# Performance work log

Measured on AMD Instinct MI355X. Metric: run time of the kernel, lower is better.

## Reference

```python
import jax, jax.numpy as jnp
import numpy as np

EMBED_DIM = 768
NUM_HEADS = 12
HEAD_DIM = EMBED_DIM // NUM_HEADS
SCALE = HEAD_DIM ** -0.5


def setup_inputs() -> dict:
    key = jax.random.key(0)
    k_x, k_qw, k_qb, k_pw, k_pb = jax.random.split(key, 5)
    B, N, C = 8, 1024, EMBED_DIM
    std = C ** -0.5
    return {
        "x": jax.random.normal(k_x, (B, N, C), dtype=jnp.float32),
        "qkv_w": jax.random.normal(k_qw, (C, 3 * C), dtype=jnp.float32) * std,
        "qkv_b": jax.random.normal(k_qb, (3 * C,), dtype=jnp.float32) * 0.02,
        "proj_w": jax.random.normal(k_pw, (C, C), dtype=jnp.float32) * std,
        "proj_b": jax.random.normal(k_pb, (C,), dtype=jnp.float32) * 0.02,
    }


def reference(x, qkv_w, qkv_b, proj_w, proj_b):
    B, N, C = x.shape
    # QKV projection: [B,N,3C] -> [3,B,H,N,Dh]
    qkv = (x @ qkv_w + qkv_b).reshape(B, N, 3, NUM_HEADS, HEAD_DIM)
    qkv = jnp.transpose(qkv, (2, 0, 3, 1, 4))
    q, k, v = qkv[0], qkv[1], qkv[2]
    # attention scores [B,H,N,N]
    attn = jnp.einsum("bhqd,bhkd->bhqk", q, k) * SCALE
    attn_weights = jax.nn.softmax(attn, axis=-1)
    # dropout=0.0 (eval) -> identity
    out = jnp.einsum("bhqk,bhkd->bhqd", attn_weights, v)
    out = jnp.transpose(out, (0, 2, 1, 3)).reshape(B, N, C)
    out = out @ proj_w + proj_b
    return out, attn_weights
```

## Files before the change

kernel.cpp:

```cpp
#include <hip/hip_runtime.h>
#include <cstdint>
#include <cstddef>

namespace {

constexpr int B = 8, NSEQ = 1024, C = 768, H = 12, D = 64, N3 = 2304;
constexpr float SCALE = 0.125f;
constexpr size_t QKV_ELEMS = (size_t)B * H * NSEQ * D;

using f32x4 = __attribute__((ext_vector_type(4))) float;
using s16x8 = __attribute__((ext_vector_type(8))) short;

__device__ __forceinline__ unsigned short f2bf(float f) {
  union { float f; uint32_t u; } v; v.f = f;
  const uint32_t r = v.u + 0x7FFFu + ((v.u >> 16) & 1u);
  return (unsigned short)(r >> 16);
}
__device__ __forceinline__ float bf2f(unsigned short s) {
  union { uint32_t u; float f; } v; v.u = ((uint32_t)s) << 16;
  return v.f;
}
__device__ __forceinline__ void gload_lds16(const void* g, void* l) {
  __builtin_amdgcn_global_load_lds(
      (const __attribute__((address_space(1))) uint32_t*)g,
      (__attribute__((address_space(3))) uint32_t*)l, 16, 0, 0);
}

__global__ __launch_bounds__(256)
void cvt_x(const float* __restrict__ x, unsigned short* __restrict__ xb, int n4) {
  const int stride = gridDim.x * 256;
  for (int idx = blockIdx.x * 256 + threadIdx.x; idx < n4; idx += stride) {
    const float4 v = ((const float4*)x)[idx];
    ushort4 o;
    o.x = f2bf(v.x); o.y = f2bf(v.y); o.z = f2bf(v.z); o.w = f2bf(v.w);
    ((ushort4*)xb)[idx] = o;
  }
}

__global__ __launch_bounds__(256)
void transp_cvt(const float* __restrict__ w, unsigned short* __restrict__ wt,
                int K, int N) {
  __shared__ float t[32][33];
  const int n0 = blockIdx.x << 5, k0 = blockIdx.y << 5;
  const int tid = threadIdx.x;
  #pragma unroll
  for (int r = 0; r < 4; ++r) {
    const int e = (r << 8) + tid;
    const int kk = e >> 5, nn = e & 31;
    t[kk][nn] = w[(size_t)(k0 + kk) * N + n0 + nn];
  }
  __syncthreads();
  #pragma unroll
  for (int r = 0; r < 4; ++r) {
    const int e = (r << 8) + tid;
    const int nn = e >> 5, kk = e & 31;
    wt[(size_t)(n0 + nn) * K + k0 + kk] = f2bf(t[kk][nn]);
  }
}

template<int MODE>
__global__ __launch_bounds__(256, 2)
void gemm_bf16(const unsigned short* __restrict__ A,
               const unsigned short* __restrict__ Wt,
               const float* __restrict__ bias,
               unsigned short* __restrict__ qp, unsigned short* __restrict__ kp,
               unsigned short* __restrict__ vt, float* __restrict__ out32,
               int N, int NT) {
  constexpr int K = 768;
  __shared__ short As[128 * 64];
  __shared__ short Bs[128 * 64];
  const int tid = threadIdx.x;
  const int wid = tid >> 6, lane = tid & 63;
  const int wm = wid >> 1, wn = wid & 1;
  const int lg = lane >> 4, lr = lane & 15;

  const int cpx = gridDim.x >> 3;
  const int logical = (blockIdx.x & 7) * cpx + (blockIdx.x >> 3);
  const int bx = logical % NT, by = logical / NT;
  const int m0 = by << 7, n0 = bx << 7;

  f32x4 acc[4][4] = {};

  for (int k0 = 0; k0 < K; k0 += 64) {
    __syncthreads();
    #pragma unroll
    for (int r = 0; r < 4; ++r) {
      const int c = (r << 8) + tid;
      const int row = c >> 3, g8 = c & 7;
      const int gp = g8 ^ (row & 7);
      const int ldsoff = (((r << 8) + (wid << 6)) << 3);
      gload_lds16(A + (size_t)(m0 + row) * K + k0 + (gp << 3), (void*)(As + ldsoff));
      gload_lds16(Wt + (size_t)(n0 + row) * K + k0 + (gp << 3), (void*)(Bs + ldsoff));
    }
    __syncthreads();
    #pragma unroll
    for (int kc = 0; kc < 2; ++kc) {
      s16x8 af[4], bf[4];
      #pragma unroll
      for (int i = 0; i < 4; ++i) {
        const int ra = (wm << 6) + (i << 4) + lr;
        const int ca = ((kc << 2) + lg) ^ (ra & 7);
        af[i] = *(const s16x8*)(As + (ra << 6) + (ca << 3));
        const int rb = (wn << 6) + (i << 4) + lr;
        const int cb = ((kc << 2) + lg) ^ (rb & 7);
        bf[i] = *(const s16x8*)(Bs + (rb << 6) + (cb << 3));
      }
      #pragma unroll
      for (int i = 0; i < 4; ++i)
        #pragma unroll
        for (int j = 0; j < 4; ++j)
          acc[i][j] = __builtin_amdgcn_mfma_f32_16x16x32_bf16(af[i], bf[j], acc[i][j], 0, 0, 0);
    }
  }

  #pragma unroll
  for (int i = 0; i < 4; ++i) {
    const int m = m0 + (wm << 6) + (i << 4) + (lg << 2);
    #pragma unroll
    for (int j = 0; j < 4; ++j) {
      const int n = n0 + (wn << 6) + (j << 4) + lr;
      const float bv = bias[n];
      if (MODE == 0) {
        const int which = (n >= 1536) ? 2 : (n >= 768 ? 1 : 0);
        const int hh = (n - which * 768) >> 6;
        const int d = n & 63;
        const int b = m >> 10, ns = m & 1023;
        const size_t bh = (size_t)b * H + hh;
        if (which < 2) {
          unsigned short* dst = (which == 0 ? qp : kp) + (bh * NSEQ + ns) * D + d;
          #pragma unroll
          for (int rg = 0; rg < 4; ++rg)
            dst[(size_t)rg * D] = f2bf(acc[i][j][rg] + bv);
        } else {
          ushort4 pk;
          pk.x = f2bf(acc[i][j][0] + bv);
          pk.y = f2bf(acc[i][j][1] + bv);
          pk.z = f2bf(acc[i][j][2] + bv);
          pk.w = f2bf(acc[i][j][3] + bv);
          *(ushort4*)(vt + (bh * D + d) * NSEQ + ns) = pk;
        }
      } else {
        float* dst = out32 + (size_t)m * N + n;
        #pragma unroll
        for (int rg = 0; rg < 4; ++rg)
          dst[(size_t)rg * N] = acc[i][j][rg] + bv;
      }
    }
  }
}

constexpr int RS = 1032;

__global__ __launch_bounds__(512, 4)
void attn_mfma(const unsigned short* __restrict__ qg,
               const unsigned short* __restrict__ kg,
               const unsigned short* __restrict__ vtg,
               float* __restrict__ attnw,
               unsigned short* __restrict__ aout) {
  __shared__ short sc[32][RS];
  __shared__ float invs[32];
  const int tid = threadIdx.x;
  const int wid = tid >> 6, lane = tid & 63;
  const int lg = lane >> 4, lr = lane & 15;
  const int wq = wid >> 2, ws = wid & 3;

  const int logical = (blockIdx.x & 7) * 384 + (blockIdx.x >> 3);
  const int bh = logical >> 5;
  const int q0 = (logical & 31) << 5;
  const size_t kvbase = (size_t)bh * NSEQ * D;

  s16x8 qf[2];
  #pragma unroll
  for (int kc = 0; kc < 2; ++kc)
    qf[kc] = *(const s16x8*)(qg + kvbase + (size_t)(q0 + (wq << 4) + lr) * D + (kc << 5) + (lg << 3));

  {
    const unsigned short* kptr = kg + kvbase + (size_t)((ws << 4) + lr) * D + (lg << 3);
    #pragma unroll 4
    for (int t = 0; t < 16; ++t) {
      f32x4 cacc = {};
      #pragma unroll
      for (int kc = 0; kc < 2; ++kc) {
        const s16x8 kf = *(const s16x8*)(kptr + t * 64 * D + (kc << 5));
        cacc = __builtin_amdgcn_mfma_f32_16x16x32_bf16(qf[kc], kf, cacc, 0, 0, 0);
      }
      const int jg = (t << 6) + (ws << 4) + lr;
      #pragma unroll
      for (int rg = 0; rg < 4; ++rg)
        sc[(wq << 4) + (lg << 2) + rg][jg] = (short)f2bf(cacc[rg] * SCALE);
    }
  }
  __syncthreads();

  {
    const int row = tid >> 4, ql = tid & 15;
    float mx = -3.0e38f;
    #pragma unroll
    for (int c = 0; c < 8; ++c) {
      const s16x8 v = *(const s16x8*)(&sc[row][(ql << 3) + (c << 7)]);
      #pragma unroll
      for (int e = 0; e < 8; ++e) mx = fmaxf(mx, bf2f((unsigned short)v[e]));
    }
    #pragma unroll
    for (int off = 8; off > 0; off >>= 1) mx = fmaxf(mx, __shfl_xor(mx, off, 16));
    float s = 0.f;
    #pragma unroll
    for (int c = 0; c < 8; ++c) {
      s16x8 v = *(s16x8*)(&sc[row][(ql << 3) + (c << 7)]);
      #pragma unroll
      for (int e = 0; e < 8; ++e) {
        const float ev = __expf(bf2f((unsigned short)v[e]) - mx);
        s += ev;
        v[e] = (short)f2bf(ev);
      }
      *(s16x8*)(&sc[row][(ql << 3) + (c << 7)]) = v;
    }
    #pragma unroll
    for (int off = 8; off > 0; off >>= 1) s += __shfl_xor(s, off, 16);
    if (ql == 0) invs[row] = 1.0f / s;
  }
  __syncthreads();

  f32x4 oa0 = {}, oa1 = {};
  {
    const unsigned short* vptr = vtg + kvbase + (size_t)((ws << 4) + lr) * NSEQ + (lg << 3);
    const short* prow = &sc[(wq << 4) + lr][lg << 3];
    #pragma unroll 2
    for (int t = 0; t < 8; ++t) {
      #pragma unroll
      for (int kc = 0; kc < 2; ++kc) {
        const s16x8 va = *(const s16x8*)(vptr + (t << 7) + (kc << 5));
        const s16x8 pa = *(const s16x8*)(prow + (t << 7) + (kc << 5));
        oa0 = __builtin_amdgcn_mfma_f32_16x16x32_bf16(pa, va, oa0, 0, 0, 0);
        const s16x8 vb = *(const s16x8*)(vptr + (t << 7) + 64 + (kc << 5));
        const s16x8 pb = *(const s16x8*)(prow + (t << 7) + 64 + (kc << 5));
        oa1 = __builtin_amdgcn_mfma_f32_16x16x32_bf16(pb, vb, oa1, 0, 0, 0);
      }
    }
  }

  {
    const int b = bh / H, hh = bh - b * H;
    const int d = (ws << 4) + lr;
    #pragma unroll
    for (int rg = 0; rg < 4; ++rg) {
      const int qi = (wq << 4) + (lg << 2) + rg;
      aout[((size_t)b * NSEQ + q0 + qi) * C + hh * D + d] =
          f2bf((oa0[rg] + oa1[rg]) * invs[qi]);
    }
  }

  {
    float* wbase = attnw + ((size_t)bh * NSEQ + q0) * NSEQ;
    #pragma unroll
    for (int r = 0; r < 8; ++r) {
      const int row = (r << 2) + (tid >> 7);
      const int colb = (tid & 127) << 3;
      const float iv = invs[row];
      const s16x8 e8 = *(const s16x8*)(&sc[row][colb]);
      f32x4 o0, o1;
      o0[0] = bf2f((unsigned short)e8[0]) * iv; o0[1] = bf2f((unsigned short)e8[1]) * iv;
      o0[2] = bf2f((unsigned short)e8[2]) * iv; o0[3] = bf2f((unsigned short)e8[3]) * iv;
      o1[0] = bf2f((unsigned short)e8[4]) * iv; o1[1] = bf2f((unsigned short)e8[5]) * iv;
      o1[2] = bf2f((unsigned short)e8[6]) * iv; o1[3] = bf2f((unsigned short)e8[7]) * iv;
      __builtin_nontemporal_store(o0, (f32x4*)(wbase + (size_t)row * NSEQ + colb));
      __builtin_nontemporal_store(o1, (f32x4*)(wbase + (size_t)row * NSEQ + colb + 4));
    }
  }
}

}

extern "C" void kernel_launch(void* const* d_in, const int* in_sizes, int n_in,
                              void* d_out, int out_size, void* d_ws, size_t ws_size,
                              hipStream_t stream) {
  const float* x      = (const float*)d_in[0];
  const float* qkv_w  = (const float*)d_in[1];
  const float* qkv_b  = (const float*)d_in[2];
  const float* proj_w = (const float*)d_in[3];
  const float* proj_b = (const float*)d_in[4];

  float* out   = (float*)d_out;
  float* attnw = out + (size_t)B * NSEQ * C;

  unsigned short* xb   = (unsigned short*)d_ws;
  unsigned short* wtq  = xb   + (size_t)8192 * 768;
  unsigned short* wtp  = wtq  + (size_t)2304 * 768;
  unsigned short* qp   = wtp  + (size_t)768 * 768;
  unsigned short* kp   = qp   + QKV_ELEMS;
  unsigned short* vtp  = kp   + QKV_ELEMS;
  unsigned short* wsao = vtp  + QKV_ELEMS;

  cvt_x<<<1024, 256, 0, stream>>>(x, xb, (int)((size_t)8192 * 768 / 4));
  transp_cvt<<<dim3(N3 / 32, C / 32), 256, 0, stream>>>(qkv_w, wtq, C, N3);
  transp_cvt<<<dim3(C / 32, C / 32), 256, 0, stream>>>(proj_w, wtp, C, C);

  gemm_bf16<0><<<(N3 / 128) * (8192 / 128), 256, 0, stream>>>(
      xb, wtq, qkv_b, qp, kp, vtp, nullptr, N3, N3 / 128);

  attn_mfma<<<(NSEQ / 32) * (B * H), 512, 0, stream>>>(qp, kp, vtp, attnw, wsao);

  gemm_bf16<1><<<(C / 128) * (8192 / 128), 256, 0, stream>>>(
      wsao, wtp, proj_b, nullptr, nullptr, nullptr, out, C, C / 128);
}
```

Baseline: 292.4 us.

## Replace full-row LDS score buffer with two-pass online softmax and streaming tiles

The attention kernel no longer holds a 32x1024 bf16 score row block in LDS. A first pass runs QK^T and keeps an online max/sum per row, and the per-wave partials are merged through a small shared array. A second pass recomputes QK^T, writes the normalized weights straight to global memory and stages the exponentials in a double-buffered, XOR-swizzled 32x64 LDS tile that feeds the PV MFMA. This cuts LDS use substantially, which may allow higher occupancy. In exchange it doubles the QK^T work, adds a __syncthreads per tile, and writes the weights as scalar, non-coalesced stores instead of the vectorized nontemporal stores used before.

```diff
diff --git a/kernel.cpp b/kernel.cpp
--- a/kernel.cpp
+++ b/kernel.cpp
@@ -149,16 +149,14 @@
   }
 }
 
-constexpr int RS = 1032;
-
 __global__ __launch_bounds__(512, 4)
 void attn_mfma(const unsigned short* __restrict__ qg,
                const unsigned short* __restrict__ kg,
                const unsigned short* __restrict__ vtg,
                float* __restrict__ attnw,
                unsigned short* __restrict__ aout) {
-  __shared__ short sc[32][RS];
-  __shared__ float invs[32];
+  __shared__ short stile[2][32 * 64];
+  __shared__ float mls[4][32][2];
   const int tid = threadIdx.x;
   const int wid = tid >> 6, lane = tid & 63;
   const int lg = lane >> 4, lr = lane & 15;
@@ -174,68 +172,87 @@
   for (int kc = 0; kc < 2; ++kc)
     qf[kc] = *(const s16x8*)(qg + kvbase + (size_t)(q0 + (wq << 4) + lr) * D + (kc << 5) + (lg << 3));
 
-  {
-    const unsigned short* kptr = kg + kvbase + (size_t)((ws << 4) + lr) * D + (lg << 3);
-    #pragma unroll 4
-    for (int t = 0; t < 16; ++t) {
-      f32x4 cacc = {};
-      #pragma unroll
-      for (int kc = 0; kc < 2; ++kc) {
-        const s16x8 kf = *(const s16x8*)(kptr + t * 64 * D + (kc << 5));
-        cacc = __builtin_amdgcn_mfma_f32_16x16x32_bf16(qf[kc], kf, cacc, 0, 0, 0);
-      }
-      const int jg = (t << 6) + (ws << 4) + lr;
-      #pragma unroll
-      for (int rg = 0; rg < 4; ++rg)
-        sc[(wq << 4) + (lg << 2) + rg][jg] = (short)f2bf(cacc[rg] * SCALE);
+  const unsigned short* kptr = kg + kvbase + (size_t)((ws << 4) + lr) * D + (lg << 3);
+
+  float M[4] = {-3.0e38f, -3.0e38f, -3.0e38f, -3.0e38f};
+  float L[4] = {0.f, 0.f, 0.f, 0.f};
+  #pragma unroll 4
+  for (int t = 0; t < 16; ++t) {
+    f32x4 cacc = {};
+    #pragma unroll
+    for (int kc = 0; kc < 2; ++kc) {
+      const s16x8 kf = *(const s16x8*)(kptr + t * 64 * D + (kc << 5));
+      cacc = __builtin_amdgcn_mfma_f32_16x16x32_bf16(qf[kc], kf, cacc, 0, 0, 0);
+    }
+    #pragma unroll
+    for (int rg = 0; rg < 4; ++rg) {
+      const float s = cacc[rg] * SCALE;
+      const float mo = M[rg];
+      const float mn = fmaxf(mo, s);
+      M[rg] = mn;
+      L[rg] = L[rg] * __expf(mo - mn) + __expf(s - mn);
+    }
+  }
+  #pragma unroll
+  for (int off = 1; off < 16; off <<= 1) {
+    #pragma unroll
+    for (int rg = 0; rg < 4; ++rg) {
+      const float m2 = __shfl_xor(M[rg], off, 16);
+      const float l2 = __shfl_xor(L[rg], off, 16);
+      const float mn = fmaxf(M[rg], m2);
+      L[rg] = L[rg] * __expf(M[rg] - mn) + l2 * __expf(m2 - mn);
+      M[rg] = mn;
+    }
+  }
+  if (lr == 0) {
+    #pragma unroll
+    for (int rg = 0; rg < 4; ++rg) {
+      mls[ws][(wq << 4) + (lg << 2) + rg][0] = M[rg];
+      mls[ws][(wq << 4) + (lg << 2) + rg][1] = L[rg];
     }
   }
   __syncthreads();
-
-  {
-    const int row = tid >> 4, ql = tid & 15;
-    float mx = -3.0e38f;
-    #pragma unroll
-    for (int c = 0; c < 8; ++c) {
-      const s16x8 v = *(const s16x8*)(&sc[row][(ql << 3) + (c << 7)]);
-      #pragma unroll
-      for (int e = 0; e < 8; ++e) mx = fmaxf(mx, bf2f((unsigned short)v[e]));
-    }
-    #pragma unroll
-    for (int off = 8; off > 0; off >>= 1) mx = fmaxf(mx, __shfl_xor(mx, off, 16));
-    float s = 0.f;
-    #pragma unroll
-    for (int c = 0; c < 8; ++c) {
-      s16x8 v = *(s16x8*)(&sc[row][(ql << 3) + (c << 7)]);
-      #pragma unroll
-      for (int e = 0; e < 8; ++e) {
-        const float ev = __expf(bf2f((unsigned short)v[e]) - mx);
-        s += ev;
-        v[e] = (short)f2bf(ev);
-      }
-      *(s16x8*)(&sc[row][(ql << 3) + (c << 7)]) = v;
-    }
-    #pragma unroll
-    for (int off = 8; off > 0; off >>= 1) s += __shfl_xor(s, off, 16);
-    if (ql == 0) invs[row] = 1.0f / s;
-  }
-  __syncthreads();
-
-  f32x4 oa0 = {}, oa1 = {};
-  {
-    const unsigned short* vptr = vtg + kvbase + (size_t)((ws << 4) + lr) * NSEQ + (lg << 3);
-    const short* prow = &sc[(wq << 4) + lr][lg << 3];
-    #pragma unroll 2
-    for (int t = 0; t < 8; ++t) {
-      #pragma unroll
-      for (int kc = 0; kc < 2; ++kc) {
-        const s16x8 va = *(const s16x8*)(vptr + (t << 7) + (kc << 5));
-        const s16x8 pa = *(const s16x8*)(prow + (t << 7) + (kc << 5));
-        oa0 = __builtin_amdgcn_mfma_f32_16x16x32_bf16(pa, va, oa0, 0, 0, 0);
-        const s16x8 vb = *(const s16x8*)(vptr + (t << 7) + 64 + (kc << 5));
-        const s16x8 pb = *(const s16x8*)(prow + (t << 7) + 64 + (kc << 5));
-        oa1 = __builtin_amdgcn_mfma_f32_16x16x32_bf16(pb, vb, oa1, 0, 0, 0);
-      }
+  float invL[4];
+  #pragma unroll
+  for (int rg = 0; rg < 4; ++rg) {
+    const int q = (wq << 4) + (lg << 2) + rg;
+    const float mf = fmaxf(fmaxf(mls[0][q][0], mls[1][q][0]),
+                           fmaxf(mls[2][q][0], mls[3][q][0]));
+    float lf = 0.f;
+    #pragma unroll
+    for (int w = 0; w < 4; ++w)
+      lf += mls[w][q][1] * __expf(mls[w][q][0] - mf);
+    M[rg] = mf;
+    invL[rg] = 1.0f / lf;
+  }
+
+  f32x4 oacc = {};
+  const unsigned short* vptr = vtg + kvbase + (size_t)((ws << 4) + lr) * NSEQ + (lg << 3);
+  float* wrow = attnw + ((size_t)bh * NSEQ + q0 + (wq << 4) + (lg << 2)) * NSEQ + (ws << 4) + lr;
+  const int prow = (wq << 4) + lr;
+
+  for (int t = 0; t < 16; ++t) {
+    f32x4 cacc = {};
+    #pragma unroll
+    for (int kc = 0; kc < 2; ++kc) {
+      const s16x8 kf = *(const s16x8*)(kptr + t * 64 * D + (kc << 5));
+      cacc = __builtin_amdgcn_mfma_f32_16x16x32_bf16(qf[kc], kf, cacc, 0, 0, 0);
+    }
+    short* sb = &stile[t & 1][0];
+    #pragma unroll
+    for (int rg = 0; rg < 4; ++rg) {
+      const float e = __expf(cacc[rg] * SCALE - M[rg]);
+      wrow[(size_t)rg * NSEQ + (t << 6)] = e * invL[rg];
+      const int q = (wq << 4) + (lg << 2) + rg;
+      sb[(q << 6) + (((ws << 4) + lr) ^ ((q & 7) << 3))] = (short)f2bf(e);
+    }
+    __syncthreads();
+    const short* sr = &stile[t & 1][prow << 6];
+    #pragma unroll
+    for (int kc = 0; kc < 2; ++kc) {
+      const s16x8 pa = *(const s16x8*)(sr + (((kc << 5) + (lg << 3)) ^ ((lr & 7) << 3)));
+      const s16x8 vf = *(const s16x8*)(vptr + (t << 6) + (kc << 5));
+      oacc = __builtin_amdgcn_mfma_f32_16x16x32_bf16(pa, vf, oacc, 0, 0, 0);
     }
   }
 
@@ -245,26 +262,7 @@
     #pragma unroll
     for (int rg = 0; rg < 4; ++rg) {
       const int qi = (wq << 4) + (lg << 2) + rg;
-      aout[((size_t)b * NSEQ + q0 + qi) * C + hh * D + d] =
-          f2bf((oa0[rg] + oa1[rg]) * invs[qi]);
-    }
-  }
-
-  {
-    float* wbase = attnw + ((size_t)bh * NSEQ + q0) * NSEQ;
-    #pragma unroll
-    for (int r = 0; r < 8; ++r) {
-      const int row = (r << 2) + (tid >> 7);
-      const int colb = (tid & 127) << 3;
-      const float iv = invs[row];
-      const s16x8 e8 = *(const s16x8*)(&sc[row][colb]);
-      f32x4 o0, o1;
-      o0[0] = bf2f((unsigned short)e8[0]) * iv; o0[1] = bf2f((unsigned short)e8[1]) * iv;
-      o0[2] = bf2f((unsigned short)e8[2]) * iv; o0[3] = bf2f((unsigned short)e8[3]) * iv;
-      o1[0] = bf2f((unsigned short)e8[4]) * iv; o1[1] = bf2f((unsigned short)e8[5]) * iv;
-      o1[2] = bf2f((unsigned short)e8[6]) * iv; o1[3] = bf2f((unsigned short)e8[7]) * iv;
-      __builtin_nontemporal_store(o0, (f32x4*)(wbase + (size_t)row * NSEQ + colb));
-      __builtin_nontemporal_store(o1, (f32x4*)(wbase + (size_t)row * NSEQ + colb + 4));
+      aout[((size_t)b * NSEQ + q0 + qi) * C + hh * D + d] = f2bf(oacc[rg] * invL[rg]);
     }
   }
 }
```

After: 364.1 us. 24.5% more time.

## Swizzle score LDS layout, transpose QK MFMA, interleave attn-weight stores into PV loop

Applied to the files above, without the earlier changes.

The QK^T MFMA now has its operands swapped, so each lane holds four consecutive key columns and writes them as one packed 8-byte LDS store instead of four scattered 2-byte stores. The score buffer uses an XOR swizzle on 8-element chunks to cut LDS bank conflicts on the writes, the softmax reads and the PV operand reads. The float attention-weight writeout is folded into the PV loop so global stores overlap the MFMA work, and the nontemporal hint is dropped. The PV loop also now walks 64-column steps with one V fragment per kc, which changes how the global V loads are issued.

```diff
diff --git a/kernel.cpp b/kernel.cpp
--- a/kernel.cpp
+++ b/kernel.cpp
@@ -151,13 +151,17 @@
 
 constexpr int RS = 1032;
 
+__device__ __forceinline__ int scidx(int q, int col) {
+  return q * RS + ((((col >> 3) ^ (q & 7)) << 3) | (col & 7));
+}
+
 __global__ __launch_bounds__(512, 4)
 void attn_mfma(const unsigned short* __restrict__ qg,
                const unsigned short* __restrict__ kg,
                const unsigned short* __restrict__ vtg,
                float* __restrict__ attnw,
                unsigned short* __restrict__ aout) {
-  __shared__ short sc[32][RS];
+  __shared__ __align__(16) short sc[32 * RS];
   __shared__ float invs[32];
   const int tid = threadIdx.x;
   const int wid = tid >> 6, lane = tid & 63;
@@ -176,28 +180,30 @@
 
   {
     const unsigned short* kptr = kg + kvbase + (size_t)((ws << 4) + lr) * D + (lg << 3);
+    const int qloc = (wq << 4) + lr;
     #pragma unroll 4
     for (int t = 0; t < 16; ++t) {
-      f32x4 cacc = {};
+      f32x4 acc = {};
       #pragma unroll
       for (int kc = 0; kc < 2; ++kc) {
         const s16x8 kf = *(const s16x8*)(kptr + t * 64 * D + (kc << 5));
-        cacc = __builtin_amdgcn_mfma_f32_16x16x32_bf16(qf[kc], kf, cacc, 0, 0, 0);
-      }
-      const int jg = (t << 6) + (ws << 4) + lr;
-      #pragma unroll
-      for (int rg = 0; rg < 4; ++rg)
-        sc[(wq << 4) + (lg << 2) + rg][jg] = (short)f2bf(cacc[rg] * SCALE);
+        acc = __builtin_amdgcn_mfma_f32_16x16x32_bf16(kf, qf[kc], acc, 0, 0, 0);
+      }
+      ushort4 pk;
+      pk.x = f2bf(acc[0] * SCALE); pk.y = f2bf(acc[1] * SCALE);
+      pk.z = f2bf(acc[2] * SCALE); pk.w = f2bf(acc[3] * SCALE);
+      *(ushort4*)(sc + scidx(qloc, (t << 6) + (ws << 4) + (lg << 2))) = pk;
     }
   }
   __syncthreads();
 
   {
     const int row = tid >> 4, ql = tid & 15;
+    const int rx = row & 7;
     float mx = -3.0e38f;
     #pragma unroll
     for (int c = 0; c < 8; ++c) {
-      const s16x8 v = *(const s16x8*)(&sc[row][(ql << 3) + (c << 7)]);
+      const s16x8 v = *(const s16x8*)(sc + row * RS + (((ql + (c << 4)) ^ rx) << 3));
       #pragma unroll
       for (int e = 0; e < 8; ++e) mx = fmaxf(mx, bf2f((unsigned short)v[e]));
     }
@@ -206,14 +212,14 @@
     float s = 0.f;
     #pragma unroll
     for (int c = 0; c < 8; ++c) {
-      s16x8 v = *(s16x8*)(&sc[row][(ql << 3) + (c << 7)]);
+      s16x8 v = *(s16x8*)(sc + row * RS + (((ql + (c << 4)) ^ rx) << 3));
       #pragma unroll
       for (int e = 0; e < 8; ++e) {
         const float ev = __expf(bf2f((unsigned short)v[e]) - mx);
         s += ev;
         v[e] = (short)f2bf(ev);
       }
-      *(s16x8*)(&sc[row][(ql << 3) + (c << 7)]) = v;
+      *(s16x8*)(sc + row * RS + (((ql + (c << 4)) ^ rx) << 3)) = v;
     }
     #pragma unroll
     for (int off = 8; off > 0; off >>= 1) s += __shfl_xor(s, off, 16);
@@ -223,19 +229,28 @@
 
   f32x4 oa0 = {}, oa1 = {};
   {
-    const unsigned short* vptr = vtg + kvbase + (size_t)((ws << 4) + lr) * NSEQ + (lg << 3);
-    const short* prow = &sc[(wq << 4) + lr][lg << 3];
-    #pragma unroll 2
-    for (int t = 0; t < 8; ++t) {
+    const int qrow = (wq << 4) + lr;
+    const int srow = tid >> 4;
+    const float sinv = invs[srow];
+    const unsigned short* vptr = vtg + ((size_t)bh * D + (ws << 4) + lr) * NSEQ + (lg << 3);
+    float* wrow = attnw + ((size_t)bh * NSEQ + q0 + srow) * NSEQ;
+    const int qx = qrow & 7;
+
+    for (int t = 0; t < 16; ++t) {
+      const int j0 = t << 6;
       #pragma unroll
       for (int kc = 0; kc < 2; ++kc) {
-        const s16x8 va = *(const s16x8*)(vptr + (t << 7) + (kc << 5));
-        const s16x8 pa = *(const s16x8*)(prow + (t << 7) + (kc << 5));
-        oa0 = __builtin_amdgcn_mfma_f32_16x16x32_bf16(pa, va, oa0, 0, 0, 0);
-        const s16x8 vb = *(const s16x8*)(vptr + (t << 7) + 64 + (kc << 5));
-        const s16x8 pb = *(const s16x8*)(prow + (t << 7) + 64 + (kc << 5));
-        oa1 = __builtin_amdgcn_mfma_f32_16x16x32_bf16(pb, vb, oa1, 0, 0, 0);
-      }
+        const s16x8 pa = *(const s16x8*)(sc + qrow * RS + ((((j0 >> 3) + (kc << 2) + lg) ^ qx) << 3));
+        const s16x8 vf = *(const s16x8*)(vptr + j0 + (kc << 5));
+        if (kc == 0) oa0 = __builtin_amdgcn_mfma_f32_16x16x32_bf16(pa, vf, oa0, 0, 0, 0);
+        else         oa1 = __builtin_amdgcn_mfma_f32_16x16x32_bf16(pa, vf, oa1, 0, 0, 0);
+      }
+      const int scol = j0 + ((tid & 15) << 2);
+      const ushort4 e4 = *(const ushort4*)(sc + srow * RS + ((((scol >> 3) ^ (srow & 7)) << 3) | (scol & 7)));
+      f32x4 w;
+      w[0] = bf2f(e4.x) * sinv; w[1] = bf2f(e4.y) * sinv;
+      w[2] = bf2f(e4.z) * sinv; w[3] = bf2f(e4.w) * sinv;
+      *(f32x4*)(wrow + scol) = w;
     }
   }
 
@@ -247,24 +262,6 @@
       const int qi = (wq << 4) + (lg << 2) + rg;
       aout[((size_t)b * NSEQ + q0 + qi) * C + hh * D + d] =
           f2bf((oa0[rg] + oa1[rg]) * invs[qi]);
-    }
-  }
-
-  {
-    float* wbase = attnw + ((size_t)bh * NSEQ + q0) * NSEQ;
-    #pragma unroll
-    for (int r = 0; r < 8; ++r) {
-      const int row = (r << 2) + (tid >> 7);
-      const int colb = (tid & 127) << 3;
-      const float iv = invs[row];
-      const s16x8 e8 = *(const s16x8*)(&sc[row][colb]);
-      f32x4 o0, o1;
-      o0[0] = bf2f((unsigned short)e8[0]) * iv; o0[1] = bf2f((unsigned short)e8[1]) * iv;
-      o0[2] = bf2f((unsigned short)e8[2]) * iv; o0[3] = bf2f((unsigned short)e8[3]) * iv;
-      o1[0] = bf2f((unsigned short)e8[4]) * iv; o1[1] = bf2f((unsigned short)e8[5]) * iv;
-      o1[2] = bf2f((unsigned short)e8[6]) * iv; o1[3] = bf2f((unsigned short)e8[7]) * iv;
-      __builtin_nontemporal_store(o0, (f32x4*)(wbase + (size_t)row * NSEQ + colb));
-      __builtin_nontemporal_store(o1, (f32x4*)(wbase + (size_t)row * NSEQ + colb + 4));
     }
   }
 }
```

Result: faster. 283.2 us (-3.1%).
